# Kernel tuning notes

Measured on AMD Instinct MI355X. Metric: run time of the kernel, lower is better.

The kernel has to match this reference:

```python
import jax, jax.numpy as jnp
import numpy as np
import math

D_MODEL = 2048
N_HEADS = 16
N_KV = 4
HEAD_DIM = D_MODEL // N_HEADS          # 128
SUB = HEAD_DIM // 2                    # 64
WINDOW = 512
THETA = 10000.0
B, S = 1, 2048


def rotate_half(x):
    x1, x2 = x[..., : x.shape[-1] // 2], x[..., x.shape[-1] // 2 :]
    return jnp.concatenate([-x2, x1], axis=-1)


def setup_inputs() -> dict:
    key = jax.random.key(0)
    ks = jax.random.split(key, 6)
    std = 0.02
    x = jax.random.normal(ks[0], (B, S, D_MODEL), dtype=jnp.float32)
    Wq = jax.random.normal(ks[1], (D_MODEL, N_HEADS * HEAD_DIM), dtype=jnp.float32) * std
    Wk = jax.random.normal(ks[2], (D_MODEL, N_KV * HEAD_DIM), dtype=jnp.float32) * std
    Wv = jax.random.normal(ks[3], (D_MODEL, N_KV * HEAD_DIM), dtype=jnp.float32) * std
    Wo = jax.random.normal(ks[4], (N_HEADS * HEAD_DIM, D_MODEL), dtype=jnp.float32) * std
    lam = jnp.full((N_HEADS,), 0.1, dtype=jnp.float32)  # diff_lambda_init
    return {"x": x, "Wq": Wq, "Wk": Wk, "Wv": Wv, "Wo": Wo, "lam": lam}


def reference(x, Wq, Wk, Wv, Wo, lam):
    b, s, _ = x.shape
    # projections -> [B, H, S, hd]
    q = (x @ Wq).reshape(b, s, N_HEADS, HEAD_DIM).transpose(0, 2, 1, 3)
    k = (x @ Wk).reshape(b, s, N_KV, HEAD_DIM).transpose(0, 2, 1, 3)
    v = (x @ Wv).reshape(b, s, N_KV, HEAD_DIM).transpose(0, 2, 1, 3)

    # RoPE (position_offset = 0)
    inv_freq = 1.0 / (THETA ** (jnp.arange(0, HEAD_DIM, 2, dtype=jnp.float32) / HEAD_DIM))
    t = jnp.arange(s, dtype=jnp.float32)
    freqs = t[:, None] * inv_freq[None, :]
    emb = jnp.concatenate([freqs, freqs], axis=-1)          # [S, hd]
    cos, sin = jnp.cos(emb), jnp.sin(emb)
    q = q * cos + rotate_half(q) * sin
    k = k * cos + rotate_half(k) * sin

    # GQA: repeat-interleave kv heads (head = kv*n_rep + r)
    n_rep = N_HEADS // N_KV
    k = jnp.repeat(k, n_rep, axis=1)
    v = jnp.repeat(v, n_rep, axis=1)

    scale = 1.0 / math.sqrt(SUB)
    q1, q2 = q[..., :SUB], q[..., SUB:]
    k1, k2 = k[..., :SUB], k[..., SUB:]
    a1 = jnp.einsum("bhqd,bhkd->bhqk", q1, k1) * scale
    a2 = jnp.einsum("bhqd,bhkd->bhqk", q2, k2) * scale

    # causal + sliding-window mask
    row = jnp.arange(s)[:, None]
    col = jnp.arange(s)[None, :]
    allowed = (col <= row) & (col >= row - WINDOW + 1)
    neg = jnp.where(allowed, 0.0, -jnp.inf).astype(a1.dtype)
    a1 = a1 + neg
    a2 = a2 + neg

    p1 = jax.nn.softmax(a1.astype(jnp.float32), axis=-1).astype(x.dtype)
    p2 = jax.nn.softmax(a2.astype(jnp.float32), axis=-1).astype(x.dtype)

    diff = jax.nn.relu(p1 - lam[None, :, None, None] * p2)
    diff = diff / (diff.sum(axis=-1, keepdims=True) + 1e-6)

    out = jnp.einsum("bhqk,bhkd->bhqd", diff, v)            # [B,H,S,hd]
    out = out.transpose(0, 2, 1, 3).reshape(b, s, N_HEADS * HEAD_DIM)
    return out @ Wo
```

## Files before the change

kernel.cpp:

```cpp
#include <hip/hip_runtime.h>

typedef unsigned short u16;
typedef __attribute__((ext_vector_type(8))) short s8b;
typedef __attribute__((ext_vector_type(4))) float f4;
typedef __attribute__((ext_vector_type(8))) _Float16 h8;

static __device__ __forceinline__ float b2f(u16 u){
  return __uint_as_float(((unsigned int)u) << 16);
}
static __device__ __forceinline__ u16 f2b(float f){
  unsigned int u = __float_as_uint(f);
  u = (u + 0x7FFFu + ((u >> 16) & 1u)) >> 16;
  return (u16)u;
}
static __device__ __forceinline__ f4 mfma16(s8b a, s8b b, f4 c){
  return __builtin_amdgcn_mfma_f32_16x16x32_bf16(a, b, c, 0, 0, 0);
}
static __device__ __forceinline__ s8b load8(const float* p){
  float4 a = ((const float4*)p)[0];
  float4 b = ((const float4*)p)[1];
  s8b r;
  r[0] = (short)f2b(a.x); r[1] = (short)f2b(a.y);
  r[2] = (short)f2b(a.z); r[3] = (short)f2b(a.w);
  r[4] = (short)f2b(b.x); r[5] = (short)f2b(b.y);
  r[6] = (short)f2b(b.z); r[7] = (short)f2b(b.w);
  return r;
}
static __device__ __forceinline__ void gload16(const u16* g, u16* l){
  __builtin_amdgcn_global_load_lds((const __attribute__((address_space(1))) void*)g,
                                   (__attribute__((address_space(3))) void*)l,
                                   16, 0, 0);
}

__global__ void convert_k(const float* __restrict__ in, u16* __restrict__ out,
                          int n8){
  const int i = blockIdx.x * blockDim.x + threadIdx.x;
  if (i < n8) ((s8b*)out)[i] = load8(in + (size_t)i * 8);
}

__global__ void transpose_k(const float* __restrict__ in, u16* __restrict__ out,
                            int K, int N){
  __shared__ u16 tile[32][33];
  const int n0 = blockIdx.x << 5, k0 = blockIdx.y << 5;
  const int tx = threadIdx.x, ty = threadIdx.y;
  #pragma unroll
  for (int i = ty; i < 32; i += 8)
    tile[i][tx] = f2b(in[(size_t)(k0 + i) * N + n0 + tx]);
  __syncthreads();
  #pragma unroll
  for (int i = ty; i < 32; i += 8)
    out[(size_t)(n0 + i) * K + k0 + tx] = tile[tx][i];
}

__global__ void transpose3_k(const float* __restrict__ Wq,
                             const float* __restrict__ Wk,
                             const float* __restrict__ Wv,
                             u16* __restrict__ out){
  __shared__ u16 tile[32][33];
  int bx = blockIdx.x;
  const float* src; int N; int rowoff;
  if (bx < 64)      { src = Wq; N = 2048; rowoff = 0; }
  else if (bx < 80) { src = Wk; N = 512;  rowoff = 2048; bx -= 64; }
  else              { src = Wv; N = 512;  rowoff = 2560; bx -= 80; }
  const int n0 = bx << 5, k0 = blockIdx.y << 5;
  const int tx = threadIdx.x, ty = threadIdx.y;
  #pragma unroll
  for (int i = ty; i < 32; i += 8)
    tile[i][tx] = f2b(src[(size_t)(k0 + i) * N + n0 + tx]);
  __syncthreads();
  #pragma unroll
  for (int i = ty; i < 32; i += 8)
    out[(size_t)(rowoff + n0 + i) * 2048 + k0 + tx] = tile[tx][i];
}

template <int MODE>
__global__ __launch_bounds__(512) void gemm8(const u16* __restrict__ A,
                                             const u16* __restrict__ Bt,
                                             u16* __restrict__ Cq,
                                             u16* __restrict__ Ck,
                                             u16* __restrict__ Cv,
                                             float* __restrict__ Cf,
                                             int M, int K){
  __shared__ __align__(16) u16 As[2][128 * 32];
  __shared__ __align__(16) u16 Bs[2][128 * 32];
  const int n0 = blockIdx.x << 7;
  const int m0 = blockIdx.y << 7;
  const int tid = threadIdx.x;
  const int wave = tid >> 6, lane = tid & 63;
  const int quad = lane >> 4, ln = lane & 15;
  const int wr = (wave >> 2) << 6;
  const int wc = (wave & 3) << 5;
  const int lr = tid >> 2;
  const int lc = (((tid & 3) ^ ((tid >> 3) & 3)) << 3);

  f4 acc[4][2];
  #pragma unroll
  for (int i = 0; i < 4; ++i)
    #pragma unroll
    for (int j = 0; j < 2; ++j){ f4 z = {0.f,0.f,0.f,0.f}; acc[i][j] = z; }

  const u16* ag = A  + (size_t)(m0 + lr) * K + lc;
  const u16* bg = Bt + (size_t)(n0 + lr) * K + lc;
  const int NT = K >> 5;
  const int rsw = ((ln >> 1) & 3) << 3;

  gload16(ag, As[0] + tid * 8);
  gload16(bg, Bs[0] + tid * 8);

  for (int t = 0; t < NT; ++t){
    const int cur = t & 1;
    const int kn = ((t + 1) < NT ? (t + 1) : t) << 5;
    gload16(ag + kn, As[cur ^ 1] + tid * 8);
    gload16(bg + kn, Bs[cur ^ 1] + tid * 8);
    asm volatile("s_waitcnt vmcnt(2)" ::: "memory");
    __builtin_amdgcn_s_barrier();
    s8b af[4], bf[2];
    #pragma unroll
    for (int i = 0; i < 4; ++i)
      af[i] = *(const s8b*)&As[cur][(wr + i*16 + ln)*32 + ((quad*8) ^ rsw)];
    #pragma unroll
    for (int j = 0; j < 2; ++j)
      bf[j] = *(const s8b*)&Bs[cur][(wc + j*16 + ln)*32 + ((quad*8) ^ rsw)];
    #pragma unroll
    for (int i = 0; i < 4; ++i)
      #pragma unroll
      for (int j = 0; j < 2; ++j)
        acc[i][j] = mfma16(af[i], bf[j], acc[i][j]);
    asm volatile("s_waitcnt lgkmcnt(0)" ::: "memory");
    __builtin_amdgcn_s_barrier();
  }
  #pragma unroll
  for (int i = 0; i < 4; ++i)
    #pragma unroll
    for (int j = 0; j < 2; ++j)
      #pragma unroll
      for (int r = 0; r < 4; ++r){
        const int row = m0 + wr + i*16 + quad*4 + r;
        const int col = n0 + wc + j*16 + ln;
        const float v = acc[i][j][r];
        if (MODE == 1){
          Cf[(size_t)row * 2048 + col] = v;
        } else {
          if (col < 2048)       Cq[(size_t)row * 2048 + col]          = f2b(v);
          else if (col < 2560)  Ck[(size_t)row * 512  + (col - 2048)] = f2b(v);
          else                  Cv[(size_t)(col - 2560) * 2048 + row] = f2b(v);
        }
      }
}

__global__ void rope2_k(u16* __restrict__ q, u16* __restrict__ k){
  const int s = blockIdx.x;
  #pragma unroll
  for (int it = 0; it < 5; ++it){
    const int p = it * 256 + threadIdx.x;
    int hh, i; u16* base;
    if (p < 1024){
      hh = p >> 6; i = p & 63;
      base = q + (size_t)s * 2048 + hh * 128 + i;
    } else {
      const int pp = p - 1024;
      hh = pp >> 6; i = pp & 63;
      base = k + (size_t)s * 512 + hh * 128 + i;
    }
    const float inv = __expf(-(float)i * 0.14391157f);
    const float ang = (float)s * inv;
    float c, sn;
    sincosf(ang, &sn, &c);
    const float x1 = b2f(base[0]), x2 = b2f(base[64]);
    base[0]  = f2b(x1 * c - x2 * sn);
    base[64] = f2b(x2 * c + x1 * sn);
  }
}

__global__ __launch_bounds__(256) void attn_k(const u16* __restrict__ q,
                                              const u16* __restrict__ kk,
                                              const u16* __restrict__ vt,
                                              const float* __restrict__ lam,
                                              u16* __restrict__ ctx){
  const int h   = blockIdx.x >> 5;
  const int qt  = blockIdx.x & 31;
  const int qt0 = qt << 6;
  const int tid = threadIdx.x;
  const int w = tid >> 6, lane = tid & 63;
  const int quad = lane >> 4, ln = lane & 15;
  const int kvh = h >> 2;
  const float lam_h = lam[h];
  const float scale = 0.125f;
  const int qbw = qt0 + (w << 4);

  __shared__ __align__(16) u16 Ks[2][32 * 128];
  __shared__ __align__(16) u16 Vs[2][128 * 32];
  __shared__ __align__(16) u16 p_lds[4][2][16][40];

  s8b qf[4];
  {
    const u16* qrow = q + (size_t)(qbw + ln) * 2048 + h * 128 + quad * 8;
    #pragma unroll
    for (int s = 0; s < 4; ++s) qf[s] = *(const s8b*)(qrow + s * 32);
  }

  const int tlo = (qt0 > 511) ? ((qt0 - 511) >> 5) : 0;
  const int thi = ((qt0 + 63) >> 5) + 1;

#define STAGE_K(buf, t) {                                                         \
    const int kc = (t) << 5;                                                      \
    _Pragma("unroll")                                                             \
    for (int i_ = 0; i_ < 2; ++i_){                                               \
      const int slot = tid + i_ * 256;                                            \
      const int row_ = slot >> 4, c16_ = slot & 15;                               \
      const u16* src_ = kk + (size_t)(kc + row_) * 512 + kvh * 128                \
                        + ((c16_ ^ (row_ & 7)) << 3);                             \
      gload16(src_, &Ks[buf][slot * 8]);                                          \
    } }
#define STAGE_V(buf, t) {                                                         \
    const int kc = (t) << 5;                                                      \
    _Pragma("unroll")                                                             \
    for (int i_ = 0; i_ < 2; ++i_){                                               \
      const int slot = tid + i_ * 256;                                            \
      const int row_ = slot >> 2, c16_ = slot & 3;                                \
      const u16* src_ = vt + (size_t)(kvh * 128 + row_) * 2048 + kc               \
                        + ((c16_ ^ ((row_ >> 1) & 3)) << 3);                      \
      gload16(src_, &Vs[buf][slot * 8]);                                          \
    } }

  h8 eh[18], eh2[18];
  float l1[4] = {0.f,0.f,0.f,0.f}, l2[4] = {0.f,0.f,0.f,0.f};

  STAGE_K(0, tlo);
  asm volatile("s_waitcnt vmcnt(0)" ::: "memory");
  __builtin_amdgcn_s_barrier();
  #pragma unroll
  for (int tt = 0; tt < 18; ++tt){
    const int t = tlo + tt;
    if (t >= thi) continue;
    const int cur = tt & 1;
    if (t + 1 < thi){
      STAGE_K(cur ^ 1, t + 1);
      asm volatile("s_waitcnt vmcnt(2)" ::: "memory");
    } else {
      asm volatile("s_waitcnt vmcnt(0)" ::: "memory");
    }
    __builtin_amdgcn_s_barrier();
    const int kcol0 = t << 5;
    if (kcol0 <= qbw + 15 && kcol0 + 31 >= qbw - 511){
      #pragma unroll
      for (int sub = 0; sub < 2; ++sub){
        const int krow = (sub*16 + ln) * 128;
        s8b kf0 = *(const s8b*)&Ks[cur][krow + (((quad +  0) ^ (ln & 7)) << 3)];
        s8b kf1 = *(const s8b*)&Ks[cur][krow + (((quad +  4) ^ (ln & 7)) << 3)];
        s8b kf2 = *(const s8b*)&Ks[cur][krow + (((quad +  8) ^ (ln & 7)) << 3)];
        s8b kf3 = *(const s8b*)&Ks[cur][krow + (((quad + 12) ^ (ln & 7)) << 3)];
        f4 z = {0.f,0.f,0.f,0.f};
        f4 s1 = mfma16(qf[1], kf1, mfma16(qf[0], kf0, z));
        f4 s2 = mfma16(qf[3], kf3, mfma16(qf[2], kf2, z));
        const int col = kcol0 + sub*16 + ln;
        h8 ev;
        #pragma unroll
        for (int r = 0; r < 4; ++r){
          const int row = qbw + quad*4 + r;
          const bool ok = (col <= row) && (col > row - 512);
          const float a = ok ? __expf(s1[r] * scale) * 0.0625f : 0.f;
          const float b = ok ? __expf(s2[r] * scale) * 0.0625f : 0.f;
          l1[r] += a; l2[r] += b;
          ev[2*r]   = (_Float16)a;
          ev[2*r+1] = (_Float16)b;
        }
        if (sub == 0) eh[tt] = ev; else eh2[tt] = ev;
      }
    }
    asm volatile("s_waitcnt lgkmcnt(0)" ::: "memory");
    __builtin_amdgcn_s_barrier();
  }
  #pragma unroll
  for (int r = 0; r < 4; ++r){
    #pragma unroll
    for (int off = 1; off < 16; off <<= 1){
      l1[r] += __shfl_xor(l1[r], off, 16);
      l2[r] += __shfl_xor(l2[r], off, 16);
    }
  }
  float il1[4], il2[4];
  #pragma unroll
  for (int r = 0; r < 4; ++r){ il1[r] = 1.f / l1[r]; il2[r] = 1.f / l2[r]; }

  f4 acc[8];
  #pragma unroll
  for (int dt = 0; dt < 8; ++dt){ f4 z = {0.f,0.f,0.f,0.f}; acc[dt] = z; }
  float den[4] = {0.f,0.f,0.f,0.f};

  STAGE_V(0, tlo);
  asm volatile("s_waitcnt vmcnt(0)" ::: "memory");
  __builtin_amdgcn_s_barrier();
  #pragma unroll
  for (int tt = 0; tt < 18; ++tt){
    const int t = tlo + tt;
    if (t >= thi) continue;
    const int cur = tt & 1;
    if (t + 1 < thi){
      STAGE_V(cur ^ 1, t + 1);
      asm volatile("s_waitcnt vmcnt(2)" ::: "memory");
    } else {
      asm volatile("s_waitcnt vmcnt(0)" ::: "memory");
    }
    __builtin_amdgcn_s_barrier();
    const int kcol0 = t << 5;
    if (kcol0 <= qbw + 15 && kcol0 + 31 >= qbw - 511){
      #pragma unroll
      for (int sub = 0; sub < 2; ++sub){
        const h8 ev = (sub == 0) ? eh[tt] : eh2[tt];
        #pragma unroll
        for (int r = 0; r < 4; ++r){
          const float a = (float)ev[2*r];
          const float b = (float)ev[2*r+1];
          const float pd = fmaxf(a * il1[r] - lam_h * (b * il2[r]), 0.f);
          den[r] += pd;
          p_lds[w][cur][quad*4 + r][sub*16 + ln] = f2b(pd);
        }
      }
      s8b pf = *(const s8b*)&p_lds[w][cur][ln][quad * 8];
      #pragma unroll
      for (int dt = 0; dt < 8; ++dt){
        s8b vf = *(const s8b*)&Vs[cur][(dt*16 + ln)*32 + (((quad) ^ ((ln >> 1) & 3)) << 3)];
        acc[dt] = mfma16(pf, vf, acc[dt]);
      }
    }
    asm volatile("s_waitcnt lgkmcnt(0)" ::: "memory");
    __builtin_amdgcn_s_barrier();
  }

  #pragma unroll
  for (int r = 0; r < 4; ++r)
    #pragma unroll
    for (int off = 1; off < 16; off <<= 1)
      den[r] += __shfl_xor(den[r], off, 16);
  #pragma unroll
  for (int r = 0; r < 4; ++r){
    const float dn = 1.f / (den[r] + 1e-6f);
    const int row = qbw + quad*4 + r;
    u16* orow = ctx + (size_t)row * 2048 + h * 128 + ln;
    #pragma unroll
    for (int dt = 0; dt < 8; ++dt)
      orow[dt * 16] = f2b(acc[dt][r] * dn);
  }
#undef STAGE_K
#undef STAGE_V
}

extern "C" void kernel_launch(void* const* d_in, const int* in_sizes, int n_in,
                              void* d_out, int out_size, void* d_ws, size_t ws_size,
                              hipStream_t stream){
  (void)in_sizes; (void)n_in; (void)out_size; (void)ws_size;
  const float* x   = (const float*)d_in[0];
  const float* Wq  = (const float*)d_in[1];
  const float* Wk  = (const float*)d_in[2];
  const float* Wv  = (const float*)d_in[3];
  const float* Wo  = (const float*)d_in[4];
  const float* lam = (const float*)d_in[5];
  char* ws = (char*)d_ws;
  u16* WT  = (u16*)(ws);
  u16* kb  = (u16*)(ws + (size_t)(13u << 20));
  u16* vtb = (u16*)(ws + (size_t)(15u << 20));
  u16* ctx = WT;
  u16* WoT = (u16*)(ws + (size_t)( 8u << 20));
  u16* xb  = (u16*)d_out;
  u16* qb  = (u16*)((char*)d_out + (size_t)(8u << 20));
  float* out = (float*)d_out;

  const dim3 tb(32, 8);
  convert_k<<<2048, 256, 0, stream>>>(x, xb, 2048 * 2048 / 8);
  transpose3_k<<<dim3(96, 64), tb, 0, stream>>>(Wq, Wk, Wv, WT);
  gemm8<0><<<dim3(24, 16), 512, 0, stream>>>(xb, WT, qb, kb, vtb, nullptr, 2048, 2048);
  rope2_k<<<2048, 256, 0, stream>>>(qb, kb);
  attn_k<<<512, 256, 0, stream>>>(qb, kb, vtb, lam, ctx);
  transpose_k<<<dim3(64, 64), tb, 0, stream>>>(Wo, WoT, 2048, 2048);
  gemm8<1><<<dim3(16, 16), 512, 0, stream>>>(ctx, WoT, nullptr, nullptr, nullptr, out, 2048, 2048);
}
```

Baseline: 242.7 us.

## Fuse RoPE into QKV GEMM epilogue and merge input conversion kernels

```diff
diff --git a/kernel.cpp b/kernel.cpp
--- a/kernel.cpp
+++ b/kernel.cpp
@@ -32,10 +32,32 @@
                                    16, 0, 0);
 }
 
-__global__ void convert_k(const float* __restrict__ in, u16* __restrict__ out,
-                          int n8){
-  const int i = blockIdx.x * blockDim.x + threadIdx.x;
-  if (i < n8) ((s8b*)out)[i] = load8(in + (size_t)i * 8);
+__global__ void prep_k(const float* __restrict__ x, u16* __restrict__ xb,
+                       const float* __restrict__ Wq, const float* __restrict__ Wk,
+                       const float* __restrict__ Wv, u16* __restrict__ WT){
+  __shared__ u16 tile[32][33];
+  const int bx = blockIdx.x;
+  if (bx < 2048){
+    const int i = bx * 256 + threadIdx.x;
+    ((s8b*)xb)[i] = load8(x + (size_t)i * 8);
+    return;
+  }
+  const int b2 = bx - 2048;
+  int nb = b2 % 96;
+  const int kb_ = b2 / 96;
+  const float* src; int N; int rowoff;
+  if (nb < 64)      { src = Wq; N = 2048; rowoff = 0; }
+  else if (nb < 80) { src = Wk; N = 512;  rowoff = 2048; nb -= 64; }
+  else              { src = Wv; N = 512;  rowoff = 2560; nb -= 80; }
+  const int n0 = nb << 5, k0 = kb_ << 5;
+  const int tx = threadIdx.x & 31, ty = threadIdx.x >> 5;
+  #pragma unroll
+  for (int i = ty; i < 32; i += 8)
+    tile[i][tx] = f2b(src[(size_t)(k0 + i) * N + n0 + tx]);
+  __syncthreads();
+  #pragma unroll
+  for (int i = ty; i < 32; i += 8)
+    WT[(size_t)(rowoff + n0 + i) * 2048 + k0 + tx] = tile[tx][i];
 }
 
 __global__ void transpose_k(const float* __restrict__ in, u16* __restrict__ out,
@@ -50,27 +72,6 @@
   #pragma unroll
   for (int i = ty; i < 32; i += 8)
     out[(size_t)(n0 + i) * K + k0 + tx] = tile[tx][i];
-}
-
-__global__ void transpose3_k(const float* __restrict__ Wq,
-                             const float* __restrict__ Wk,
-                             const float* __restrict__ Wv,
-                             u16* __restrict__ out){
-  __shared__ u16 tile[32][33];
-  int bx = blockIdx.x;
-  const float* src; int N; int rowoff;
-  if (bx < 64)      { src = Wq; N = 2048; rowoff = 0; }
-  else if (bx < 80) { src = Wk; N = 512;  rowoff = 2048; bx -= 64; }
-  else              { src = Wv; N = 512;  rowoff = 2560; bx -= 80; }
-  const int n0 = bx << 5, k0 = blockIdx.y << 5;
-  const int tx = threadIdx.x, ty = threadIdx.y;
-  #pragma unroll
-  for (int i = ty; i < 32; i += 8)
-    tile[i][tx] = f2b(src[(size_t)(k0 + i) * N + n0 + tx]);
-  __syncthreads();
-  #pragma unroll
-  for (int i = ty; i < 32; i += 8)
-    out[(size_t)(rowoff + n0 + i) * 2048 + k0 + tx] = tile[tx][i];
 }
 
 template <int MODE>
@@ -81,8 +82,7 @@
                                              u16* __restrict__ Cv,
                                              float* __restrict__ Cf,
                                              int M, int K){
-  __shared__ __align__(16) u16 As[2][128 * 32];
-  __shared__ __align__(16) u16 Bs[2][128 * 32];
+  __shared__ __align__(16) u16 smem[(MODE == 0) ? 17408 : 16384];
   const int n0 = blockIdx.x << 7;
   const int m0 = blockIdx.y << 7;
   const int tid = threadIdx.x;
@@ -104,23 +104,27 @@
   const int NT = K >> 5;
   const int rsw = ((ln >> 1) & 3) << 3;
 
-  gload16(ag, As[0] + tid * 8);
-  gload16(bg, Bs[0] + tid * 8);
+  gload16(ag, smem + tid * 8);
+  gload16(bg, smem + 8192 + tid * 8);
 
   for (int t = 0; t < NT; ++t){
     const int cur = t & 1;
-    const int kn = ((t + 1) < NT ? (t + 1) : t) << 5;
-    gload16(ag + kn, As[cur ^ 1] + tid * 8);
-    gload16(bg + kn, Bs[cur ^ 1] + tid * 8);
-    asm volatile("s_waitcnt vmcnt(2)" ::: "memory");
+    if (t + 1 < NT){
+      const int kn = (t + 1) << 5;
+      gload16(ag + kn, smem + (cur ^ 1) * 4096 + tid * 8);
+      gload16(bg + kn, smem + 8192 + (cur ^ 1) * 4096 + tid * 8);
+      asm volatile("s_waitcnt vmcnt(2)" ::: "memory");
+    } else {
+      asm volatile("s_waitcnt vmcnt(0)" ::: "memory");
+    }
     __builtin_amdgcn_s_barrier();
     s8b af[4], bf[2];
     #pragma unroll
     for (int i = 0; i < 4; ++i)
-      af[i] = *(const s8b*)&As[cur][(wr + i*16 + ln)*32 + ((quad*8) ^ rsw)];
+      af[i] = *(const s8b*)&smem[cur*4096 + (wr + i*16 + ln)*32 + ((quad*8) ^ rsw)];
     #pragma unroll
     for (int j = 0; j < 2; ++j)
-      bf[j] = *(const s8b*)&Bs[cur][(wc + j*16 + ln)*32 + ((quad*8) ^ rsw)];
+      bf[j] = *(const s8b*)&smem[8192 + cur*4096 + (wc + j*16 + ln)*32 + ((quad*8) ^ rsw)];
     #pragma unroll
     for (int i = 0; i < 4; ++i)
       #pragma unroll
@@ -129,46 +133,59 @@
     asm volatile("s_waitcnt lgkmcnt(0)" ::: "memory");
     __builtin_amdgcn_s_barrier();
   }
-  #pragma unroll
-  for (int i = 0; i < 4; ++i)
-    #pragma unroll
-    for (int j = 0; j < 2; ++j)
-      #pragma unroll
-      for (int r = 0; r < 4; ++r){
-        const int row = m0 + wr + i*16 + quad*4 + r;
-        const int col = n0 + wc + j*16 + ln;
-        const float v = acc[i][j][r];
-        if (MODE == 1){
-          Cf[(size_t)row * 2048 + col] = v;
-        } else {
-          if (col < 2048)       Cq[(size_t)row * 2048 + col]          = f2b(v);
-          else if (col < 2560)  Ck[(size_t)row * 512  + (col - 2048)] = f2b(v);
-          else                  Cv[(size_t)(col - 2560) * 2048 + row] = f2b(v);
-        }
-      }
-}
-
-__global__ void rope2_k(u16* __restrict__ q, u16* __restrict__ k){
-  const int s = blockIdx.x;
-  #pragma unroll
-  for (int it = 0; it < 5; ++it){
-    const int p = it * 256 + threadIdx.x;
-    int hh, i; u16* base;
-    if (p < 1024){
-      hh = p >> 6; i = p & 63;
-      base = q + (size_t)s * 2048 + hh * 128 + i;
-    } else {
-      const int pp = p - 1024;
-      hh = pp >> 6; i = pp & 63;
-      base = k + (size_t)s * 512 + hh * 128 + i;
-    }
-    const float inv = __expf(-(float)i * 0.14391157f);
-    const float ang = (float)s * inv;
-    float c, sn;
-    sincosf(ang, &sn, &c);
-    const float x1 = b2f(base[0]), x2 = b2f(base[64]);
-    base[0]  = f2b(x1 * c - x2 * sn);
-    base[64] = f2b(x2 * c + x1 * sn);
+
+  if (MODE == 1){
+    #pragma unroll
+    for (int i = 0; i < 4; ++i)
+      #pragma unroll
+      for (int j = 0; j < 2; ++j)
+        #pragma unroll
+        for (int r = 0; r < 4; ++r){
+          const int row = m0 + wr + i*16 + quad*4 + r;
+          const int col = n0 + wc + j*16 + ln;
+          Cf[(size_t)row * 2048 + col] = acc[i][j][r];
+        }
+  } else if (n0 >= 2560){
+    #pragma unroll
+    for (int i = 0; i < 4; ++i)
+      #pragma unroll
+      for (int j = 0; j < 2; ++j)
+        #pragma unroll
+        for (int r = 0; r < 4; ++r){
+          const int row = m0 + wr + i*16 + quad*4 + r;
+          const int col = n0 + wc + j*16 + ln;
+          Cv[(size_t)(col - 2560) * 2048 + row] = f2b(acc[i][j][r]);
+        }
+  } else {
+    #pragma unroll
+    for (int i = 0; i < 4; ++i)
+      #pragma unroll
+      for (int j = 0; j < 2; ++j)
+        #pragma unroll
+        for (int r = 0; r < 4; ++r)
+          smem[(wr + i*16 + quad*4 + r) * 136 + wc + j*16 + ln] = f2b(acc[i][j][r]);
+    asm volatile("s_waitcnt lgkmcnt(0)" ::: "memory");
+    __builtin_amdgcn_s_barrier();
+    #pragma unroll
+    for (int j = 0; j < 2; ++j){
+      const int c  = wc + j*16 + ln;
+      const int iq = c & 63;
+      const float inv = __expf(-(float)iq * 0.14391157f);
+      #pragma unroll
+      for (int i = 0; i < 4; ++i)
+        #pragma unroll
+        for (int r = 0; r < 4; ++r){
+          const int rl  = wr + i*16 + quad*4 + r;
+          const int row = m0 + rl;
+          float cs, sn;
+          sincosf((float)row * inv, &sn, &cs);
+          const float xv = b2f(smem[rl*136 + c]);
+          const float xp = b2f(smem[rl*136 + (c ^ 64)]);
+          const float res = (c < 64) ? (xv*cs - xp*sn) : (xv*cs + xp*sn);
+          if (n0 < 2048) Cq[(size_t)row * 2048 + n0 + c]          = f2b(res);
+          else           Ck[(size_t)row * 512  + (n0 - 2048) + c] = f2b(res);
+        }
+    }
   }
 }
 
@@ -367,10 +384,8 @@
   float* out = (float*)d_out;
 
   const dim3 tb(32, 8);
-  convert_k<<<2048, 256, 0, stream>>>(x, xb, 2048 * 2048 / 8);
-  transpose3_k<<<dim3(96, 64), tb, 0, stream>>>(Wq, Wk, Wv, WT);
+  prep_k<<<8192, 256, 0, stream>>>(x, xb, Wq, Wk, Wv, WT);
   gemm8<0><<<dim3(24, 16), 512, 0, stream>>>(xb, WT, qb, kb, vtb, nullptr, 2048, 2048);
-  rope2_k<<<2048, 256, 0, stream>>>(qb, kb);
   attn_k<<<512, 256, 0, stream>>>(qb, kb, vtb, lam, ctx);
   transpose_k<<<dim3(64, 64), tb, 0, stream>>>(Wo, WoT, 2048, 2048);
   gemm8<1><<<dim3(16, 16), 512, 0, stream>>>(ctx, WoT, nullptr, nullptr, nullptr, out, 2048, 2048);
```

Result: faster. 222.3 us (-8.4%).
